# Kernel tuning notes

Hardware: AMD Instinct MI355X
Metric: run time of the kernel (lower is better)

The kernel has to match this reference:

```python
import jax, jax.numpy as jnp
import numpy as np

N_NODES = 50000
N_EDGES = 800000
IN_CH = 128
HEADS = 4
HEAD_DIM = 32  # out_channels // heads = 128 // 4
OUT_CH = HEADS * HEAD_DIM
NEG_SLOPE = 0.2
LN_EPS = 1e-5


def setup_inputs() -> dict:
    key = jax.random.key(0)
    ks = jax.random.split(key, 10)
    s = 1.0 / np.sqrt(IN_CH)
    return {
        "x": jax.random.normal(ks[0], (N_NODES, IN_CH), jnp.float32),
        "edge_index": jax.random.randint(ks[1], (2, N_EDGES), 0, N_NODES, dtype=jnp.int64),
        "W_l": jax.random.normal(ks[2], (IN_CH, OUT_CH), jnp.float32) * s,
        "b_l": jnp.zeros((OUT_CH,), jnp.float32),
        "W_r": jax.random.normal(ks[3], (IN_CH, OUT_CH), jnp.float32) * s,
        "b_r": jnp.zeros((OUT_CH,), jnp.float32),
        "att": jax.random.normal(ks[4], (HEADS, HEAD_DIM), jnp.float32) * (1.0 / np.sqrt(HEAD_DIM)),
        "bias": jnp.zeros((OUT_CH,), jnp.float32),
        "gamma": jnp.ones((OUT_CH,), jnp.float32),
        "beta": jnp.zeros((OUT_CH,), jnp.float32),
    }


def reference(x, edge_index, W_l, b_l, W_r, b_r, att, bias, gamma, beta):
    N = x.shape[0]
    H, C = att.shape
    # add self loops (PyG GATv2Conv default add_self_loops=True)
    loops = jnp.arange(N, dtype=edge_index.dtype)
    src = jnp.concatenate([edge_index[0], loops])  # source j
    dst = jnp.concatenate([edge_index[1], loops])  # target i
    # separate source/target transforms (share_weights=False)
    xl = (x @ W_l + b_l).reshape(N, H, C)  # source features
    xr = (x @ W_r + b_r).reshape(N, H, C)  # target features
    # GATv2 attention: e_ij = att . leaky_relu(xl_j + xr_i)
    e = xl[src] + xr[dst]                              # [E', H, C]
    e = jnp.where(e > 0, e, NEG_SLOPE * e)             # leaky_relu(0.2)
    score = jnp.einsum('ehc,hc->eh', e, att)           # [E', H]
    # segment softmax over edges sharing the same destination node
    smax = jax.ops.segment_max(score, dst, num_segments=N)      # [N, H]
    score = jnp.exp(score - smax[dst])
    denom = jax.ops.segment_sum(score, dst, num_segments=N)     # [N, H]
    alpha = score / denom[dst]                                   # [E', H]
    # weighted scatter-sum of source messages
    msg = alpha[:, :, None] * xl[src]                            # [E', H, C]
    out = jax.ops.segment_sum(msg, dst, num_segments=N)          # [N, H, C]
    out = out.reshape(N, H * C) + bias
    # SiLU
    out = out * jax.nn.sigmoid(out)
    # LayerNorm over feature dim
    mu = jnp.mean(out, axis=-1, keepdims=True)
    var = jnp.mean(jnp.square(out - mu), axis=-1, keepdims=True)
    out = (out - mu) * jax.lax.rsqrt(var + LN_EPS) * gamma + beta
    return out
```

## Files before the change

kernel.cpp:

```cpp
#include <hip/hip_runtime.h>
#include <hip/hip_fp16.h>
#include <math.h>

#define CH 128
#define NEG_SLOPE 0.2f
#define LN_EPS 1e-5f
#define CAP 64

typedef _Float16 f16;
typedef _Float16 f16x2 __attribute__((ext_vector_type(2)));
typedef _Float16 f16x4 __attribute__((ext_vector_type(4)));
typedef _Float16 f16x8 __attribute__((ext_vector_type(8)));
typedef float    f32x4 __attribute__((ext_vector_type(4)));

__device__ __forceinline__ f16x2 u2h(unsigned u) {
    union { unsigned u; f16x2 h; } v; v.u = u; return v.h;
}

__device__ __forceinline__ float row16_allreduce(float x) {
    int t;
    t = __builtin_amdgcn_update_dpp(0, __builtin_bit_cast(int, x), 0xB1, 0xF, 0xF, false);
    x += __builtin_bit_cast(float, t);
    t = __builtin_amdgcn_update_dpp(0, __builtin_bit_cast(int, x), 0x4E, 0xF, 0xF, false);
    x += __builtin_bit_cast(float, t);
    t = __builtin_amdgcn_update_dpp(0, __builtin_bit_cast(int, x), 0x141, 0xF, 0xF, false);
    x += __builtin_bit_cast(float, t);
    t = __builtin_amdgcn_update_dpp(0, __builtin_bit_cast(int, x), 0x140, 0xF, 0xF, false);
    x += __builtin_bit_cast(float, t);
    return x;
}

__global__ void k_init(const float* __restrict__ Wl, const float* __restrict__ Wr,
                       f16* __restrict__ Wt, int* __restrict__ cnt, int N)
{
    int tid = blockIdx.x * 256 + threadIdx.x;
    if (tid < 256 * CH) {
        int k   = tid >> 8;
        int col = tid & 255;
        float w = (col < CH) ? Wl[k * CH + col] : Wr[k * CH + (col - CH)];
        Wt[(size_t)col * CH + k] = (f16)w;
    }
    if (tid < N) cnt[tid] = 0;
}

__global__ __launch_bounds__(256) void k_transform(
    const float* __restrict__ x, const f16* __restrict__ Wt,
    const float* __restrict__ bl, const float* __restrict__ br,
    f16* __restrict__ xlh, f16* __restrict__ xrh, int N)
{
    const int wave = (blockIdx.x * 256 + threadIdx.x) >> 6;
    const int lane = threadIdx.x & 63;
    const int m0   = wave * 16;
    if (m0 >= N) return;

    const int n16  = lane & 15;
    const int quad = lane >> 4;

    f16x8 xfr[4];
    {
        int mrow = m0 + n16; if (mrow >= N) mrow = N - 1;
        const float* xrow = x + (size_t)mrow * CH + quad * 8;
#pragma unroll
        for (int ks = 0; ks < 4; ++ks) {
            float4 p0 = *(const float4*)(xrow + ks * 32);
            float4 p1 = *(const float4*)(xrow + ks * 32 + 4);
            f16x8 f; f[0] = (f16)p0.x; f[1] = (f16)p0.y; f[2] = (f16)p0.z; f[3] = (f16)p0.w;
                     f[4] = (f16)p1.x; f[5] = (f16)p1.y; f[6] = (f16)p1.z; f[7] = (f16)p1.w;
            xfr[ks] = f;
        }
    }

#pragma unroll
    for (int ct = 0; ct < 16; ++ct) {
        f32x4 acc = {0.f, 0.f, 0.f, 0.f};
        const int acol = ct * 16 + n16;
        const f16* wp = Wt + (size_t)acol * CH + quad * 8;
#pragma unroll
        for (int ks = 0; ks < 4; ++ks) {
            f16x8 afr = *(const f16x8*)(wp + ks * 32);
            acc = __builtin_amdgcn_mfma_f32_16x16x32_f16(afr, xfr[ks], acc, 0, 0, 0);
        }
        const int node = m0 + n16;
        const int chq  = ct * 16 + quad * 4;
        if (node < N) {
            if (ct < 8) {
                float4 bv = *(const float4*)&bl[chq];
                f16x4 pk = {(f16)(acc[0] + bv.x), (f16)(acc[1] + bv.y),
                            (f16)(acc[2] + bv.z), (f16)(acc[3] + bv.w)};
                *(f16x4*)(xlh + (size_t)node * CH + chq) = pk;
            } else {
                int cc = chq - CH;
                float4 bv = *(const float4*)&br[cc];
                f16x4 pk = {(f16)(acc[0] + bv.x), (f16)(acc[1] + bv.y),
                            (f16)(acc[2] + bv.z), (f16)(acc[3] + bv.w)};
                *(f16x4*)(xrh + (size_t)node * CH + cc) = pk;
            }
        }
    }
}

#define FILL_EPB 4096
__global__ __launch_bounds__(256) void k_fill(
    const int* __restrict__ ei, int E, unsigned CM,
    int* __restrict__ cnt, int* __restrict__ col)
{
    const int cls = blockIdx.x & 7;
    const int sl  = blockIdx.x >> 3;
    const int base = sl * FILL_EPB + threadIdx.x * 4;

#pragma unroll
    for (int i = 0; i < 4; ++i) {
        int e = base + i * 1024;
        if (e < E) {
            int4 dv = *(const int4*)&ei[E + e];
            int4 sv = *(const int4*)&ei[e];
            int dd[4] = {dv.x, dv.y, dv.z, dv.w};
            int ss[4] = {sv.x, sv.y, sv.z, sv.w};
#pragma unroll
            for (int k = 0; k < 4; ++k) {
                int d = dd[k];
                if ((int)__umulhi((unsigned)d, CM) == cls) {
                    int pos = atomicAdd(&cnt[d], 1);
                    if (pos < CAP) col[((size_t)d << 6) + pos] = ss[k];
                }
            }
        }
    }
}

__global__ __launch_bounds__(256) void k_aggregate(
    const f16* __restrict__ xlh, const f16* __restrict__ xrh,
    const int* __restrict__ col, const int* __restrict__ cnt,
    const float* __restrict__ att, const float* __restrict__ bias,
    const float* __restrict__ gamma, const float* __restrict__ beta,
    float* __restrict__ out, int N)
{
    const int wid  = __builtin_amdgcn_readfirstlane(threadIdx.x >> 6);
    const int lane = threadIdx.x & 63;
    const int n    = blockIdx.x * 4 + wid;
    if (n >= N) return;

    const int start = n << 6;
    int cn = cnt[n]; cn = cn < CAP ? cn : CAP;
    const int end = start + cn;

    const int c = 2 * lane;
    f16x2 xr2, at2;
    {
        xr2 = *(const f16x2*)&xrh[(size_t)n * CH + c];
        float2 a = *(const float2*)&att[c];
        at2 = (f16x2){(f16)(a.x * 1.44269504f), (f16)(a.y * 1.44269504f)};
    }
    const f16x2 c02 = {(f16)NEG_SLOPE, (f16)NEG_SLOPE};
    const unsigned laneoff = (unsigned)c;

    float l_run, accx, accy;
    {
        unsigned us = *(const unsigned*)(xlh + ((size_t)n << 7) + laneoff);
        f16x2 u  = u2h(us);
        f16x2 tt = u + xr2;
        f16x2 lk = __builtin_elementwise_max(tt, tt * c02);
        float s  = __builtin_amdgcn_fdot2(lk, at2, 0.f, false);
        s = row16_allreduce(s);
        float w;
        asm("v_exp_f32 %0, %1" : "=v"(w) : "v"(s));
        l_run = w;
        accx  = (float)u[0] * w;
        accy  = (float)u[1] * w;
    }

    int cc[8];
#pragma unroll
    for (int k = 0; k < 8; ++k) cc[k] = col[start + k];

    for (int p = start; p < end; p += 8) {
        unsigned gv[8];
#pragma unroll
        for (int k = 0; k < 8; ++k) {
            unsigned si = (unsigned)cc[k];
            si = (si < (unsigned)N) ? si : 0u;
            gv[k] = *(const unsigned*)(xlh + ((size_t)si << 7) + laneoff);
        }
#pragma unroll
        for (int k = 0; k < 8; ++k) cc[k] = col[p + 8 + k];
#pragma unroll
        for (int k = 0; k < 8; ++k) {
            f16x2 u  = u2h(gv[k]);
            f16x2 tt = u + xr2;
            f16x2 lk = __builtin_elementwise_max(tt, tt * c02);
            float s  = __builtin_amdgcn_fdot2(lk, at2, 0.f, false);
            s = row16_allreduce(s);
            float w;
            asm("v_exp_f32 %0, %1" : "=v"(w) : "v"(s));
            w = (p + k < end) ? w : 0.f;
            l_run += w;
            accx += (float)u[0] * w;
            accy += (float)u[1] * w;
        }
    }

    const float inv = 1.f / l_run;
    float y0 = accx * inv + bias[c];
    float y1 = accy * inv + bias[c + 1];
    y0 = y0 / (1.f + __expf(-y0));
    y1 = y1 / (1.f + __expf(-y1));
    float s1 = y0 + y1;
    float s2 = y0 * y0 + y1 * y1;
#pragma unroll
    for (int off = 1; off < 64; off <<= 1) {
        s1 += __shfl_xor(s1, off);
        s2 += __shfl_xor(s2, off);
    }
    float mu   = s1 * (1.f / 128.f);
    float var  = s2 * (1.f / 128.f) - mu * mu;
    float rstd = rsqrtf(var + LN_EPS);
    float o0 = (y0 - mu) * rstd * gamma[c]     + beta[c];
    float o1 = (y1 - mu) * rstd * gamma[c + 1] + beta[c + 1];
    *(float2*)&out[(size_t)n * CH + c] = make_float2(o0, o1);
}

extern "C" void kernel_launch(void* const* d_in, const int* in_sizes, int n_in,
                              void* d_out, int out_size, void* d_ws, size_t ws_size,
                              hipStream_t stream)
{
    const float* x    = (const float*)d_in[0];
    const int*   ei   = (const int*)  d_in[1];
    const float* Wl   = (const float*)d_in[2];
    const float* bl   = (const float*)d_in[3];
    const float* Wr   = (const float*)d_in[4];
    const float* br   = (const float*)d_in[5];
    const float* att  = (const float*)d_in[6];
    const float* bias = (const float*)d_in[7];
    const float* gam  = (const float*)d_in[8];
    const float* bet  = (const float*)d_in[9];
    float* out = (float*)d_out;

    const int N = in_sizes[0] / CH;
    const int E = in_sizes[1] / 2;

    char* ws = (char*)d_ws;
    size_t off = 0;
    auto carve = [&](size_t bytes) -> char* {
        char* p = ws + off;
        off += (bytes + 255) & ~(size_t)255;
        return p;
    };
    f16* xlh  = (f16*)carve((size_t)N * CH * sizeof(f16));
    f16* xrh  = (f16*)carve((size_t)N * CH * sizeof(f16));
    f16* Wt   = (f16*)carve((size_t)256 * CH * sizeof(f16));
    int* cnt  = (int*)carve((size_t)N * sizeof(int));
    int* col  = (int*)carve(((size_t)N * CAP + 16) * sizeof(int));
    (void)ws_size;

    const int nwaves = (N + 15) / 16;
    const int TB     = (nwaves * 64 + 255) / 256;
    const int IB     = (((N > 256 * CH ? N : 256 * CH) + 255) / 256);

    const unsigned CM = (unsigned)(((8ULL << 32) + (unsigned)N - 1) / (unsigned)N);
    const int S  = (E + FILL_EPB - 1) / FILL_EPB;
    const int FB = 8 * S;

    k_init      <<<IB, 256, 0, stream>>>(Wl, Wr, Wt, cnt, N);
    k_transform <<<TB, 256, 0, stream>>>(x, Wt, bl, br, xlh, xrh, N);
    k_fill      <<<FB, 256, 0, stream>>>(ei, E, CM, cnt, col);
    k_aggregate <<<(N + 3) / 4, 256, 0, stream>>>(xlh, xrh, col, cnt,
                                                  att, bias, gam, bet, out, N);
}
```

Before: 209.9 us.

## Process four edges per wave with 16-byte per-lane gathers in aggregation

Restructures the aggregation kernel so each wave splits into four 16-lane groups. Each group handles a different edge, and each lane gathers 8 fp16 channels (16 bytes) instead of 2. This cuts the per-edge reduction to two DPP steps and raises bytes per load instruction. Partial sums are merged with cross-group shuffles at the end. In exchange the edge loop loses its deep 8-way prefetch unrolling, which may reduce memory-level parallelism, and register use rises because of the 8 accumulators.

```diff
diff --git a/kernel.cpp b/kernel.cpp
--- a/kernel.cpp
+++ b/kernel.cpp
@@ -15,19 +15,6 @@
 
 __device__ __forceinline__ f16x2 u2h(unsigned u) {
     union { unsigned u; f16x2 h; } v; v.u = u; return v.h;
-}
-
-__device__ __forceinline__ float row16_allreduce(float x) {
-    int t;
-    t = __builtin_amdgcn_update_dpp(0, __builtin_bit_cast(int, x), 0xB1, 0xF, 0xF, false);
-    x += __builtin_bit_cast(float, t);
-    t = __builtin_amdgcn_update_dpp(0, __builtin_bit_cast(int, x), 0x4E, 0xF, 0xF, false);
-    x += __builtin_bit_cast(float, t);
-    t = __builtin_amdgcn_update_dpp(0, __builtin_bit_cast(int, x), 0x141, 0xF, 0xF, false);
-    x += __builtin_bit_cast(float, t);
-    t = __builtin_amdgcn_update_dpp(0, __builtin_bit_cast(int, x), 0x140, 0xF, 0xF, false);
-    x += __builtin_bit_cast(float, t);
-    return x;
 }
 
 __global__ void k_init(const float* __restrict__ Wl, const float* __restrict__ Wr,
@@ -140,83 +127,108 @@
     const int n    = blockIdx.x * 4 + wid;
     if (n >= N) return;
 
+    const int l16 = lane & 15;
+    const int g   = lane >> 4;
+    const int c0  = l16 * 8;
+
     const int start = n << 6;
     int cn = cnt[n]; cn = cn < CAP ? cn : CAP;
-    const int end = start + cn;
-
-    const int c = 2 * lane;
-    f16x2 xr2, at2;
+    const int total = cn + 1;
+
+    f16x8 xr8, at8;
     {
-        xr2 = *(const f16x2*)&xrh[(size_t)n * CH + c];
-        float2 a = *(const float2*)&att[c];
-        at2 = (f16x2){(f16)(a.x * 1.44269504f), (f16)(a.y * 1.44269504f)};
-    }
-    const f16x2 c02 = {(f16)NEG_SLOPE, (f16)NEG_SLOPE};
-    const unsigned laneoff = (unsigned)c;
-
-    float l_run, accx, accy;
-    {
-        unsigned us = *(const unsigned*)(xlh + ((size_t)n << 7) + laneoff);
-        f16x2 u  = u2h(us);
-        f16x2 tt = u + xr2;
-        f16x2 lk = __builtin_elementwise_max(tt, tt * c02);
-        float s  = __builtin_amdgcn_fdot2(lk, at2, 0.f, false);
-        s = row16_allreduce(s);
+        xr8 = *(const f16x8*)(xrh + (size_t)n * CH + c0);
+        float4 a0 = *(const float4*)&att[c0];
+        float4 a1 = *(const float4*)&att[c0 + 4];
+        const float L2E = 1.44269504f;
+        at8[0]=(f16)(a0.x*L2E); at8[1]=(f16)(a0.y*L2E);
+        at8[2]=(f16)(a0.z*L2E); at8[3]=(f16)(a0.w*L2E);
+        at8[4]=(f16)(a1.x*L2E); at8[5]=(f16)(a1.y*L2E);
+        at8[6]=(f16)(a1.z*L2E); at8[7]=(f16)(a1.w*L2E);
+    }
+    const f16x8 c02 = {(f16)NEG_SLOPE,(f16)NEG_SLOPE,(f16)NEG_SLOPE,(f16)NEG_SLOPE,
+                       (f16)NEG_SLOPE,(f16)NEG_SLOPE,(f16)NEG_SLOPE,(f16)NEG_SLOPE};
+
+    float l_run = 0.f;
+    float acc[8] = {0.f,0.f,0.f,0.f,0.f,0.f,0.f,0.f};
+
+    for (int t0 = 0; t0 < total; t0 += 4) {
+        const int base = start + t0 - 1;
+        int s0 = (t0 == 0) ? n : col[base];
+        int s1 = col[base + 1];
+        int s2 = col[base + 2];
+        int s3 = col[base + 3];
+        int src = (g == 0) ? s0 : ((g == 1) ? s1 : ((g == 2) ? s2 : s3));
+        unsigned su = (unsigned)src;
+        su = (su < (unsigned)N) ? su : 0u;
+
+        f16x8 u = *(const f16x8*)(xlh + ((size_t)su << 7) + c0);
+        f16x8 tt = u + xr8;
+        f16x8 lk = __builtin_elementwise_max(tt, tt * c02);
+        union { f16x8 v; f16x2 h[4]; } L, A;
+        L.v = lk; A.v = at8;
+        float s = __builtin_amdgcn_fdot2(L.h[0], A.h[0], 0.f, false);
+        s = __builtin_amdgcn_fdot2(L.h[1], A.h[1], s, false);
+        s = __builtin_amdgcn_fdot2(L.h[2], A.h[2], s, false);
+        s = __builtin_amdgcn_fdot2(L.h[3], A.h[3], s, false);
+        int t;
+        t = __builtin_amdgcn_update_dpp(0, __builtin_bit_cast(int, s), 0xB1, 0xF, 0xF, false);
+        s += __builtin_bit_cast(float, t);
+        t = __builtin_amdgcn_update_dpp(0, __builtin_bit_cast(int, s), 0x4E, 0xF, 0xF, false);
+        s += __builtin_bit_cast(float, t);
         float w;
         asm("v_exp_f32 %0, %1" : "=v"(w) : "v"(s));
-        l_run = w;
-        accx  = (float)u[0] * w;
-        accy  = (float)u[1] * w;
-    }
-
-    int cc[8];
-#pragma unroll
-    for (int k = 0; k < 8; ++k) cc[k] = col[start + k];
-
-    for (int p = start; p < end; p += 8) {
-        unsigned gv[8];
-#pragma unroll
-        for (int k = 0; k < 8; ++k) {
-            unsigned si = (unsigned)cc[k];
-            si = (si < (unsigned)N) ? si : 0u;
-            gv[k] = *(const unsigned*)(xlh + ((size_t)si << 7) + laneoff);
-        }
-#pragma unroll
-        for (int k = 0; k < 8; ++k) cc[k] = col[p + 8 + k];
-#pragma unroll
-        for (int k = 0; k < 8; ++k) {
-            f16x2 u  = u2h(gv[k]);
-            f16x2 tt = u + xr2;
-            f16x2 lk = __builtin_elementwise_max(tt, tt * c02);
-            float s  = __builtin_amdgcn_fdot2(lk, at2, 0.f, false);
-            s = row16_allreduce(s);
-            float w;
-            asm("v_exp_f32 %0, %1" : "=v"(w) : "v"(s));
-            w = (p + k < end) ? w : 0.f;
-            l_run += w;
-            accx += (float)u[0] * w;
-            accy += (float)u[1] * w;
-        }
+        w = (t0 + g < total) ? w : 0.f;
+        l_run += w;
+#pragma unroll
+        for (int j = 0; j < 8; ++j) acc[j] += (float)u[j] * w;
+    }
+
+    l_run += __shfl_xor(l_run, 16);
+    l_run += __shfl_xor(l_run, 32);
+#pragma unroll
+    for (int j = 0; j < 8; ++j) {
+        acc[j] += __shfl_xor(acc[j], 16);
+        acc[j] += __shfl_xor(acc[j], 32);
     }
 
     const float inv = 1.f / l_run;
-    float y0 = accx * inv + bias[c];
-    float y1 = accy * inv + bias[c + 1];
-    y0 = y0 / (1.f + __expf(-y0));
-    y1 = y1 / (1.f + __expf(-y1));
-    float s1 = y0 + y1;
-    float s2 = y0 * y0 + y1 * y1;
-#pragma unroll
-    for (int off = 1; off < 64; off <<= 1) {
+    float4 b0 = *(const float4*)&bias[c0];
+    float4 b1 = *(const float4*)&bias[c0 + 4];
+    float y[8];
+    y[0] = acc[0]*inv + b0.x; y[1] = acc[1]*inv + b0.y;
+    y[2] = acc[2]*inv + b0.z; y[3] = acc[3]*inv + b0.w;
+    y[4] = acc[4]*inv + b1.x; y[5] = acc[5]*inv + b1.y;
+    y[6] = acc[6]*inv + b1.z; y[7] = acc[7]*inv + b1.w;
+    float s1 = 0.f, s2 = 0.f;
+#pragma unroll
+    for (int j = 0; j < 8; ++j) {
+        y[j] = y[j] / (1.f + __expf(-y[j]));
+        s1 += y[j];
+        s2 += y[j] * y[j];
+    }
+#pragma unroll
+    for (int off = 1; off < 16; off <<= 1) {
         s1 += __shfl_xor(s1, off);
         s2 += __shfl_xor(s2, off);
     }
     float mu   = s1 * (1.f / 128.f);
     float var  = s2 * (1.f / 128.f) - mu * mu;
     float rstd = rsqrtf(var + LN_EPS);
-    float o0 = (y0 - mu) * rstd * gamma[c]     + beta[c];
-    float o1 = (y1 - mu) * rstd * gamma[c + 1] + beta[c + 1];
-    *(float2*)&out[(size_t)n * CH + c] = make_float2(o0, o1);
+    float4 g0 = *(const float4*)&gamma[c0];
+    float4 g1 = *(const float4*)&gamma[c0 + 4];
+    float4 e0 = *(const float4*)&beta[c0];
+    float4 e1 = *(const float4*)&beta[c0 + 4];
+    float4 o0, o1;
+    o0.x = (y[0]-mu)*rstd*g0.x + e0.x;  o0.y = (y[1]-mu)*rstd*g0.y + e0.y;
+    o0.z = (y[2]-mu)*rstd*g0.z + e0.z;  o0.w = (y[3]-mu)*rstd*g0.w + e0.w;
+    o1.x = (y[4]-mu)*rstd*g1.x + e1.x;  o1.y = (y[5]-mu)*rstd*g1.y + e1.y;
+    o1.z = (y[6]-mu)*rstd*g1.z + e1.z;  o1.w = (y[7]-mu)*rstd*g1.w + e1.w;
+    if (g == 0) {
+        float* orow = out + (size_t)n * CH + c0;
+        *(float4*)orow       = o0;
+        *(float4*)(orow + 4) = o1;
+    }
 }
 
 extern "C" void kernel_launch(void* const* d_in, const int* in_sizes, int n_in,
```

After: 217.1 us. 1.03x slower.
